# Kernel tuning notes

Hardware: AMD Instinct MI355X
Metric: run time of the kernel (lower is better)

The kernel has to match this reference:

```python
import jax, jax.numpy as jnp
import numpy as np

N_ATOMS = 200_000
N_PAIRS = 20_000_000
N_SPECIES = 4
N_EDGES = 101  # -> 100 bins
R_MAX_GEN = 6.5  # generate some distances beyond the last edge (they are dropped)


def setup_inputs() -> dict:
    key = jax.random.key(0)
    k1, k2, k3, k4 = jax.random.split(key, 4)
    pair_dist = jax.random.uniform(k1, (N_PAIRS,), dtype=jnp.float32) * R_MAX_GEN
    pair_first = jax.random.randint(k2, (N_PAIRS,), 0, N_ATOMS)
    pair_second = jax.random.randint(k3, (N_PAIRS,), 0, N_ATOMS)
    # strict one-hot species encoding per atom (matches hippynn's one_hot input)
    species = jax.random.randint(k4, (N_ATOMS,), 0, N_SPECIES)
    one_hot = species[:, None] == jnp.arange(N_SPECIES)[None, :]
    bins = jnp.linspace(0.0, 6.0, N_EDGES).astype(jnp.float32)  # buffer from __init__
    return {
        "pair_dist": pair_dist,
        "pair_first": pair_first,
        "pair_second": pair_second,
        "one_hot": one_hot,
        "n_molecules": 512,
        "bins": bins,
    }


def reference(pair_dist, pair_first, pair_second, one_hot, n_molecules, bins):
    # Original: for each species pair (i,j), mask pairs where one_hot[pair_first,i]
    # and one_hot[pair_second,j], then histogram masked distances into `bins` via
    # broadcast-compare + diff of counts:  count in bin b = #(bins[b] <= d < bins[b+1]).
    # Fused single-pass equivalent: bucketize each pair distance and scatter-add
    # into a flat (species_i, species_j, bin) histogram.
    n_species = one_hot.shape[-1]
    n_bins = bins.shape[0] - 1

    species = jnp.argmax(one_hot, axis=-1)          # [n_atoms], one-hot -> label
    si = species[pair_first]                        # [n_pairs]
    sj = species[pair_second]                       # [n_pairs]

    # searchsorted(side='right') - 1 gives b s.t. bins[b] <= d < bins[b+1]
    b = jnp.searchsorted(bins, pair_dist, side="right") - 1
    valid = (b >= 0) & (b < n_bins)                 # drop d < bins[0] or d >= bins[-1]
    b_safe = jnp.clip(b, 0, n_bins - 1)

    flat_idx = (si * n_species + sj) * n_bins + b_safe
    weights = valid.astype(pair_dist.dtype)
    rdf = jnp.zeros((n_species * n_species * n_bins,), dtype=pair_dist.dtype)
    rdf = rdf.at[flat_idx].add(weights)
    rdf = rdf.reshape(n_species, n_species, n_bins)
    return (rdf / n_molecules)[None]                # [1, S, S, n_bins]
```

## Files before the change

### kernel.cpp

```cpp
#include <hip/hip_runtime.h>
#include <stdint.h>


#define NSPEC 4
#define HIST_BLOCKS 512

__device__ inline int esize_from_nzw(unsigned int nzw) {
    if (nzw >= 640) return 1;
    if (nzw >= 192) return 4;
    return 8;
}

__device__ inline int get_species(const uint8_t* oh, int atom, int E) {
    if (E == 1) {
        uint32_t v = *(const uint32_t*)(oh + (size_t)atom * 4);
        if (v & 0x000000FFu) return 0;
        if (v & 0x0000FF00u) return 1;
        if (v & 0x00FF0000u) return 2;
        return 3;
    }
    const uint8_t* p = oh + (size_t)atom * 4 * E;
    for (int s = 0; s < NSPEC; ++s) {
        bool nzb = false;
        for (int b = 0; b < E; ++b) nzb |= (p[s * E + b] != 0);
        if (nzb) return s;
    }
    return 0;
}

__global__ void k_species(const uint8_t* __restrict__ oh, int n_atoms,
                          uint32_t* __restrict__ sp2,
                          unsigned int* __restrict__ counts, int n_counts) {
    __shared__ unsigned int s_nz;
    if (threadIdx.x == 0) s_nz = 0;
    __syncthreads();
    unsigned int local = 0;
    #pragma unroll
    for (int k = 0; k < 4; ++k) {
        uint32_t v = ((const uint32_t*)oh)[threadIdx.x * 4 + k];
        local += (v != 0u);
    }
    for (int off = 32; off > 0; off >>= 1) local += __shfl_down(local, off);
    if ((threadIdx.x & 63) == 0) atomicAdd(&s_nz, local);
    __syncthreads();
    const int E = esize_from_nzw(s_nz);

    const int gid = blockIdx.x * blockDim.x + threadIdx.x;
    const int gsz = gridDim.x * blockDim.x;
    for (int j = gid; j < n_counts; j += gsz) counts[j] = 0u;

    const int nw = (n_atoms + 15) >> 4;
    for (int w = gid; w < nw; w += gsz) {
        uint32_t word = 0;
        int base = w << 4;
        int lim = n_atoms - base;
        lim = lim < 16 ? lim : 16;
        for (int k = 0; k < lim; ++k)
            word |= (uint32_t)get_species(oh, base + k, E) << (k * 2);
        sp2[w] = word;
    }
}

__launch_bounds__(1024, 8) __global__
void k_hist_lds(const float* __restrict__ dist, const int* __restrict__ pf,
                const int* __restrict__ ps, const uint32_t* __restrict__ sp2,
                const float* __restrict__ bins, int n_edges, int n_words,
                int npairs, unsigned int* __restrict__ counts,
                unsigned int* __restrict__ part) {
    extern __shared__ float2 smem2[];
    const int n_bins = n_edges - 1;
    const int nh = NSPEC * NSPEC * n_bins;
    float2* eb = smem2;
    uint32_t* tab = (uint32_t*)(eb + n_bins);
    int* h = (int*)(tab + n_words);
    __shared__ int s_exact;

    const int tid = threadIdx.x;
    if (tid == 0) s_exact = 1;
    __syncthreads();

    for (int j = tid; j < n_words; j += blockDim.x) tab[j] = sp2[j];
    for (int j = tid; j < nh + 8; j += blockDim.x) h[j] = 0;
    const float lo = bins[0];
    const float hi = bins[n_edges - 1];
    const float scale = (float)n_bins / (hi - lo);

    for (int j = tid; j < n_edges; j += blockDim.x) {
        float e = bins[j];
        eb[j < n_bins ? j : 0] = make_float2(bins[j < n_bins ? j : 0],
                                             bins[(j < n_bins ? j : 0) + 1]);
        bool ok = true;
        if (j < n_bins) {
            int gi = (int)((e - lo) * scale);
            gi = gi < n_bins - 1 ? gi : n_bins - 1;
            gi = gi > 0 ? gi : 0;
            ok &= (gi == j);
        }
        if (j >= 1) {
            if (e <= 0.f) ok = false;
            else {
                float ep = __int_as_float(__float_as_int(e) - 1);
                int gi = (int)((ep - lo) * scale);
                gi = gi < n_bins - 1 ? gi : n_bins - 1;
                gi = gi > 0 ? gi : 0;
                ok &= (gi == j - 1);
            }
        }
        if (!ok) atomicAnd(&s_exact, 0);
    }
    __syncthreads();

    const int gid = blockIdx.x * blockDim.x + tid;
    const int gsz = gridDim.x * blockDim.x;
    const int nquads = npairs >> 2;
    const int dump = nh + (tid & 7);

    const float4* dist4 = (const float4*)dist;
    const int4* pf4 = (const int4*)pf;
    const int4* ps4 = (const int4*)ps;

    if (s_exact) {
        for (int q = gid; q < nquads; q += gsz) {
            float4 d4 = dist4[q];
            int4 f4 = pf4[q];
            int4 s4 = ps4[q];
            float d[4] = {d4.x, d4.y, d4.z, d4.w};
            int a0[4] = {f4.x, f4.y, f4.z, f4.w};
            int a1[4] = {s4.x, s4.y, s4.z, s4.w};
            uint32_t wi[4], wj[4];
            #pragma unroll
            for (int k = 0; k < 4; ++k) {
                wi[k] = tab[(unsigned)a0[k] >> 4];
                wj[k] = tab[(unsigned)a1[k] >> 4];
            }
            #pragma unroll
            for (int k = 0; k < 4; ++k) {
                int b = (int)((d[k] - lo) * scale);
                b = b < n_bins - 1 ? b : n_bins - 1;
                b = b > 0 ? b : 0;
                int vld = (d[k] >= lo) & (d[k] < hi);
                int si = (int)((wi[k] >> ((a0[k] & 15) << 1)) & 3u);
                int sj = (int)((wj[k] >> ((a1[k] & 15) << 1)) & 3u);
                int idx = (si * NSPEC + sj) * n_bins + b;
                atomicAdd(&h[vld ? idx : dump], 1);
            }
        }
    } else {
        for (int q = gid; q < nquads; q += gsz) {
            float4 d4 = dist4[q];
            int4 f4 = pf4[q];
            int4 s4 = ps4[q];
            float d[4] = {d4.x, d4.y, d4.z, d4.w};
            int a0[4] = {f4.x, f4.y, f4.z, f4.w};
            int a1[4] = {s4.x, s4.y, s4.z, s4.w};
            #pragma unroll
            for (int k = 0; k < 4; ++k) {
                if (d[k] >= lo && d[k] < hi) {
                    int b = (int)((d[k] - lo) * scale);
                    b = b < n_bins - 1 ? b : n_bins - 1;
                    b = b > 0 ? b : 0;
                    while (d[k] < eb[b].x) --b;
                    while (d[k] >= eb[b].y) ++b;
                    int s_i = (int)((tab[(unsigned)a0[k] >> 4] >>
                                     ((a0[k] & 15) << 1)) & 3u);
                    int s_j = (int)((tab[(unsigned)a1[k] >> 4] >>
                                     ((a1[k] & 15) << 1)) & 3u);
                    atomicAdd(&h[(s_i * NSPEC + s_j) * n_bins + b], 1);
                }
            }
        }
    }
    int tail = npairs & 3;
    if (gid < tail) {
        int i = (nquads << 2) + gid;
        float d = dist[i];
        if (d >= lo && d < hi) {
            int b = (int)((d - lo) * scale);
            b = b < n_bins - 1 ? b : n_bins - 1;
            b = b > 0 ? b : 0;
            while (d < eb[b].x) --b;
            while (d >= eb[b].y) ++b;
            int a0 = pf[i], a1 = ps[i];
            int s_i = (int)((tab[(unsigned)a0 >> 4] >> ((a0 & 15) << 1)) & 3u);
            int s_j = (int)((tab[(unsigned)a1 >> 4] >> ((a1 & 15) << 1)) & 3u);
            atomicAdd(&h[(s_i * NSPEC + s_j) * n_bins + b], 1);
        }
    }

    __syncthreads();
    if (part) {
        unsigned int* dst = part + (size_t)blockIdx.x * nh;
        for (int j = tid; j < nh; j += blockDim.x) dst[j] = (unsigned int)h[j];
    } else {
        for (int j = tid; j < nh; j += blockDim.x) {
            int v = h[j];
            if (v) atomicAdd(&counts[j], (unsigned int)v);
        }
    }
}

__launch_bounds__(256, 8) __global__
void k_hist_glb(const float* __restrict__ dist, const int* __restrict__ pf,
                const int* __restrict__ ps, const uint32_t* __restrict__ sp2,
                const float* __restrict__ bins, int n_edges, int npairs,
                unsigned int* __restrict__ counts) {
    const int n_bins = n_edges - 1;
    const int nh = NSPEC * NSPEC * n_bins;
    extern __shared__ float smem[];
    float* sb = smem;
    int* h = (int*)(smem + n_edges);
    const int tid = threadIdx.x;
    for (int j = tid; j < n_edges; j += blockDim.x) sb[j] = bins[j];
    for (int j = tid; j < nh; j += blockDim.x) h[j] = 0;
    __syncthreads();
    const float lo = sb[0];
    const float hi = sb[n_edges - 1];
    const float scale = (float)n_bins / (hi - lo);
    const int gid = blockIdx.x * blockDim.x + tid;
    const int gsz = gridDim.x * blockDim.x;
    auto species_of = [&](int a) -> int {
        return (int)((sp2[a >> 4] >> ((a & 15) << 1)) & 3u);
    };
    auto bin_and_add = [&](float d, int si, int sj) {
        if (d >= lo && d < hi) {
            int b = (int)((d - lo) * scale);
            b = b < n_bins - 1 ? b : n_bins - 1;
            b = b > 0 ? b : 0;
            while (d < sb[b]) --b;
            while (d >= sb[b + 1]) ++b;
            atomicAdd(&h[(si * NSPEC + sj) * n_bins + b], 1);
        }
    };
    const int nquads = npairs >> 2;
    for (int q = gid; q < nquads; q += gsz) {
        float4 d4 = ((const float4*)dist)[q];
        int4 f4 = ((const int4*)pf)[q];
        int4 s4 = ((const int4*)ps)[q];
        bin_and_add(d4.x, species_of(f4.x), species_of(s4.x));
        bin_and_add(d4.y, species_of(f4.y), species_of(s4.y));
        bin_and_add(d4.z, species_of(f4.z), species_of(s4.z));
        bin_and_add(d4.w, species_of(f4.w), species_of(s4.w));
    }
    int tail = npairs & 3;
    if (gid < tail) {
        int i = (nquads << 2) + gid;
        bin_and_add(dist[i], species_of(pf[i]), species_of(ps[i]));
    }
    __syncthreads();
    for (int j = tid; j < nh; j += blockDim.x) {
        int v = h[j];
        if (v) atomicAdd(&counts[j], (unsigned int)v);
    }
}

__global__ void k_reduce(const unsigned int* __restrict__ part, int nblocks,
                         int nh, const int* __restrict__ nmol,
                         float* __restrict__ out) {
    const int tid = threadIdx.x;
    const int bin = blockIdx.x * 32 + (tid >> 3);
    const int sub = tid & 7;
    if (bin >= nh) return;
    unsigned int s = 0;
    for (int k = sub; k < nblocks; k += 8) s += part[(size_t)k * nh + bin];
    s += __shfl_down(s, 4);
    s += __shfl_down(s, 2);
    s += __shfl_down(s, 1);
    if (sub == 0) out[bin] = (float)s / (float)(*nmol);
}

__global__ void k_final(const unsigned int* __restrict__ counts,
                        const int* __restrict__ nmol, float* __restrict__ out,
                        int n) {
    int i = blockIdx.x * blockDim.x + threadIdx.x;
    if (i < n) out[i] = (float)counts[i] / (float)(*nmol);
}

extern "C" void kernel_launch(void* const* d_in, const int* in_sizes, int n_in,
                              void* d_out, int out_size, void* d_ws,
                              size_t ws_size, hipStream_t stream) {
    const float* dist = (const float*)d_in[0];
    const int* pf = (const int*)d_in[1];
    const int* ps = (const int*)d_in[2];
    const uint8_t* oh = (const uint8_t*)d_in[3];
    const int* nmol = (const int*)d_in[4];
    const float* bins = (const float*)d_in[5];
    float* out = (float*)d_out;

    const int npairs = in_sizes[0];
    const int n_edges = in_sizes[5];
    const int n_bins = n_edges - 1;
    const int n_atoms = in_sizes[3] / NSPEC;
    const int nh = NSPEC * NSPEC * n_bins;

    uint8_t* ws = (uint8_t*)d_ws;
    unsigned int* counts = (unsigned int*)ws;
    uint32_t* sp2 = (uint32_t*)(ws + nh * 4 + 64);
    const int n_words = (n_atoms + 15) >> 4;
    size_t part_off = ((size_t)nh * 4 + 64 + (size_t)n_words * 4 + 255) &
                      ~(size_t)255;
    unsigned int* part = (unsigned int*)(ws + part_off);
    const size_t need_part = part_off + (size_t)HIST_BLOCKS * nh * 4;
    const bool use_tree = ws_size >= need_part;

    k_species<<<256, 256, 0, stream>>>(oh, n_atoms, sp2, counts, nh);

    const size_t shmem_lds = (size_t)n_bins * 8 + (size_t)n_words * 4 +
                             (size_t)(nh + 8) * 4;
    if (shmem_lds <= 64 * 1024) {
        k_hist_lds<<<HIST_BLOCKS, 1024, shmem_lds, stream>>>(
            dist, pf, ps, sp2, bins, n_edges, n_words, npairs, counts,
            use_tree ? part : nullptr);
    } else {
        const size_t shmem = (size_t)n_edges * 4 + (size_t)nh * 4;
        k_hist_glb<<<2048, 256, shmem, stream>>>(dist, pf, ps, sp2, bins,
                                                 n_edges, npairs, counts);
    }

    if (use_tree && shmem_lds <= 64 * 1024) {
        k_reduce<<<(nh + 31) / 32, 256, 0, stream>>>(part, HIST_BLOCKS, nh,
                                                     nmol, out);
    } else {
        k_final<<<(out_size + 255) / 256, 256, 0, stream>>>(counts, nmol, out,
                                                            out_size);
    }
}
```

Measured before the change: 89.47 us.

## Software-pipeline histogram loads three deep and drop partial-histogram tree reduction

The exact-binning loop now keeps three rounds of float4/int4 loads in flight in rotating registers, issuing the next round's loads before consuming the current one, so global memory latency overlaps with LDS atomics. Load indices past the end are clamped to the last quad so the prefetch stays in bounds. The per-block partial histogram dump and separate k_reduce kernel are removed in favour of global atomicAdd merging followed by k_final. The edge-pair table fill is also simplified into its own loop. The deeper prefetch raises register pressure, and 512 blocks contending on global atomics may cost more than the tree reduction did.

```diff
diff --git a/kernel.cpp b/kernel.cpp
--- a/kernel.cpp
+++ b/kernel.cpp
@@ -65,8 +65,7 @@
 void k_hist_lds(const float* __restrict__ dist, const int* __restrict__ pf,
                 const int* __restrict__ ps, const uint32_t* __restrict__ sp2,
                 const float* __restrict__ bins, int n_edges, int n_words,
-                int npairs, unsigned int* __restrict__ counts,
-                unsigned int* __restrict__ part) {
+                int npairs, unsigned int* __restrict__ counts) {
     extern __shared__ float2 smem2[];
     const int n_bins = n_edges - 1;
     const int nh = NSPEC * NSPEC * n_bins;
@@ -81,14 +80,14 @@
 
     for (int j = tid; j < n_words; j += blockDim.x) tab[j] = sp2[j];
     for (int j = tid; j < nh + 8; j += blockDim.x) h[j] = 0;
+    for (int j = tid; j < n_bins; j += blockDim.x)
+        eb[j] = make_float2(bins[j], bins[j + 1]);
     const float lo = bins[0];
     const float hi = bins[n_edges - 1];
     const float scale = (float)n_bins / (hi - lo);
 
     for (int j = tid; j < n_edges; j += blockDim.x) {
         float e = bins[j];
-        eb[j < n_bins ? j : 0] = make_float2(bins[j < n_bins ? j : 0],
-                                             bins[(j < n_bins ? j : 0) + 1]);
         bool ok = true;
         if (j < n_bins) {
             int gi = (int)((e - lo) * scale);
@@ -120,31 +119,73 @@
     const int4* ps4 = (const int4*)ps;
 
     if (s_exact) {
-        for (int q = gid; q < nquads; q += gsz) {
-            float4 d4 = dist4[q];
-            int4 f4 = pf4[q];
-            int4 s4 = ps4[q];
-            float d[4] = {d4.x, d4.y, d4.z, d4.w};
-            int a0[4] = {f4.x, f4.y, f4.z, f4.w};
-            int a1[4] = {s4.x, s4.y, s4.z, s4.w};
-            uint32_t wi[4], wj[4];
-            #pragma unroll
-            for (int k = 0; k < 4; ++k) {
-                wi[k] = tab[(unsigned)a0[k] >> 4];
-                wj[k] = tab[(unsigned)a1[k] >> 4];
+        const int last = nquads - 1;
+        int n_iter = 0;
+        if (gid < nquads) n_iter = (nquads - 1 - gid) / gsz + 1;
+
+        float4 dA, dB, dC;
+        int4 fA, fB, fC, sA, sB, sC;
+        int idx = gid;
+
+        #define LD(D, F, S, I)                 \
+            do {                               \
+                int c_ = (I);                  \
+                c_ = c_ < last ? c_ : last;    \
+                D = dist4[c_];                 \
+                F = pf4[c_];                   \
+                S = ps4[c_];                   \
+            } while (0)
+
+        #define CONSUME(D, F, S)                                            \
+            do {                                                            \
+                float d_[4] = {D.x, D.y, D.z, D.w};                         \
+                int a0_[4] = {F.x, F.y, F.z, F.w};                          \
+                int a1_[4] = {S.x, S.y, S.z, S.w};                          \
+                uint32_t wi_[4], wj_[4];                                    \
+                _Pragma("unroll") for (int k = 0; k < 4; ++k) {             \
+                    wi_[k] = tab[(unsigned)a0_[k] >> 4];                    \
+                    wj_[k] = tab[(unsigned)a1_[k] >> 4];                    \
+                }                                                           \
+                _Pragma("unroll") for (int k = 0; k < 4; ++k) {             \
+                    int b_ = (int)((d_[k] - lo) * scale);                   \
+                    b_ = b_ < n_bins - 1 ? b_ : n_bins - 1;                 \
+                    b_ = b_ > 0 ? b_ : 0;                                   \
+                    int vld_ = (d_[k] >= lo) & (d_[k] < hi);                \
+                    int si_ = (int)((wi_[k] >> ((a0_[k] & 15) << 1)) & 3u); \
+                    int sj_ = (int)((wj_[k] >> ((a1_[k] & 15) << 1)) & 3u); \
+                    int hx_ = (si_ * NSPEC + sj_) * n_bins + b_;            \
+                    atomicAdd(&h[vld_ ? hx_ : dump], 1);                    \
+                }                                                           \
+            } while (0)
+
+        if (n_iter > 0) {
+            LD(dA, fA, sA, idx);
+            LD(dB, fB, sB, idx + gsz);
+            LD(dC, fC, sC, idx + 2 * gsz);
+            int it = 0;
+            for (; it + 3 <= n_iter; it += 3) {
+                CONSUME(dA, fA, sA);
+                LD(dA, fA, sA, idx + 3 * gsz);
+                idx += gsz;
+                CONSUME(dB, fB, sB);
+                LD(dB, fB, sB, idx + 3 * gsz);
+                idx += gsz;
+                CONSUME(dC, fC, sC);
+                LD(dC, fC, sC, idx + 3 * gsz);
+                idx += gsz;
             }
-            #pragma unroll
-            for (int k = 0; k < 4; ++k) {
-                int b = (int)((d[k] - lo) * scale);
-                b = b < n_bins - 1 ? b : n_bins - 1;
-                b = b > 0 ? b : 0;
-                int vld = (d[k] >= lo) & (d[k] < hi);
-                int si = (int)((wi[k] >> ((a0[k] & 15) << 1)) & 3u);
-                int sj = (int)((wj[k] >> ((a1[k] & 15) << 1)) & 3u);
-                int idx = (si * NSPEC + sj) * n_bins + b;
-                atomicAdd(&h[vld ? idx : dump], 1);
+            if (it < n_iter) {
+                CONSUME(dA, fA, sA);
+                ++it;
+                if (it < n_iter) {
+                    CONSUME(dB, fB, sB);
+                    ++it;
+                    if (it < n_iter) CONSUME(dC, fC, sC);
+                }
             }
         }
+        #undef LD
+        #undef CONSUME
     } else {
         for (int q = gid; q < nquads; q += gsz) {
             float4 d4 = dist4[q];
@@ -188,14 +229,9 @@
     }
 
     __syncthreads();
-    if (part) {
-        unsigned int* dst = part + (size_t)blockIdx.x * nh;
-        for (int j = tid; j < nh; j += blockDim.x) dst[j] = (unsigned int)h[j];
-    } else {
-        for (int j = tid; j < nh; j += blockDim.x) {
-            int v = h[j];
-            if (v) atomicAdd(&counts[j], (unsigned int)v);
-        }
+    for (int j = tid; j < nh; j += blockDim.x) {
+        int v = h[j];
+        if (v) atomicAdd(&counts[j], (unsigned int)v);
     }
 }
 
@@ -253,21 +289,6 @@
     }
 }
 
-__global__ void k_reduce(const unsigned int* __restrict__ part, int nblocks,
-                         int nh, const int* __restrict__ nmol,
-                         float* __restrict__ out) {
-    const int tid = threadIdx.x;
-    const int bin = blockIdx.x * 32 + (tid >> 3);
-    const int sub = tid & 7;
-    if (bin >= nh) return;
-    unsigned int s = 0;
-    for (int k = sub; k < nblocks; k += 8) s += part[(size_t)k * nh + bin];
-    s += __shfl_down(s, 4);
-    s += __shfl_down(s, 2);
-    s += __shfl_down(s, 1);
-    if (sub == 0) out[bin] = (float)s / (float)(*nmol);
-}
-
 __global__ void k_final(const unsigned int* __restrict__ counts,
                         const int* __restrict__ nmol, float* __restrict__ out,
                         int n) {
@@ -296,11 +317,6 @@
     unsigned int* counts = (unsigned int*)ws;
     uint32_t* sp2 = (uint32_t*)(ws + nh * 4 + 64);
     const int n_words = (n_atoms + 15) >> 4;
-    size_t part_off = ((size_t)nh * 4 + 64 + (size_t)n_words * 4 + 255) &
-                      ~(size_t)255;
-    unsigned int* part = (unsigned int*)(ws + part_off);
-    const size_t need_part = part_off + (size_t)HIST_BLOCKS * nh * 4;
-    const bool use_tree = ws_size >= need_part;
 
     k_species<<<256, 256, 0, stream>>>(oh, n_atoms, sp2, counts, nh);
 
@@ -308,19 +324,13 @@
                              (size_t)(nh + 8) * 4;
     if (shmem_lds <= 64 * 1024) {
         k_hist_lds<<<HIST_BLOCKS, 1024, shmem_lds, stream>>>(
-            dist, pf, ps, sp2, bins, n_edges, n_words, npairs, counts,
-            use_tree ? part : nullptr);
+            dist, pf, ps, sp2, bins, n_edges, n_words, npairs, counts);
     } else {
         const size_t shmem = (size_t)n_edges * 4 + (size_t)nh * 4;
         k_hist_glb<<<2048, 256, shmem, stream>>>(dist, pf, ps, sp2, bins,
                                                  n_edges, npairs, counts);
     }
 
-    if (use_tree && shmem_lds <= 64 * 1024) {
-        k_reduce<<<(nh + 31) / 32, 256, 0, stream>>>(part, HIST_BLOCKS, nh,
-                                                     nmol, out);
-    } else {
-        k_final<<<(out_size + 255) / 256, 256, 0, stream>>>(counts, nmol, out,
-                                                            out_size);
-    }
-}
+    k_final<<<(out_size + 255) / 256, 256, 0, stream>>>(counts, nmol, out,
+                                                        out_size);
+}
```

Result: faster. 80.56 us (-10.0%).

## Fuse final reduction into histogram kernel via last-block atomic counter

Applied to the files above, without the earlier changes.

Replaces the per-block partial histogram write and separate reduce kernel with global atomic accumulation plus a last-block-done counter that writes the normalized output. The main loop now processes two quads per iteration so more loads are in flight, and the edge table setup is simplified. This removes one kernel launch and the partials buffer traffic. In exchange it adds global atomic contention on 1600 counters from 512 blocks and a fence-based completion check.

```diff
diff --git a/kernel.cpp b/kernel.cpp
--- a/kernel.cpp
+++ b/kernel.cpp
@@ -30,7 +30,7 @@
 
 __global__ void k_species(const uint8_t* __restrict__ oh, int n_atoms,
                           uint32_t* __restrict__ sp2,
-                          unsigned int* __restrict__ counts, int n_counts) {
+                          unsigned int* __restrict__ ws_head, int n_counts) {
     __shared__ unsigned int s_nz;
     if (threadIdx.x == 0) s_nz = 0;
     __syncthreads();
@@ -47,7 +47,7 @@
 
     const int gid = blockIdx.x * blockDim.x + threadIdx.x;
     const int gsz = gridDim.x * blockDim.x;
-    for (int j = gid; j < n_counts; j += gsz) counts[j] = 0u;
+    for (int j = gid; j < n_counts + 16; j += gsz) ws_head[j] = 0u;
 
     const int nw = (n_atoms + 15) >> 4;
     for (int w = gid; w < nw; w += gsz) {
@@ -66,7 +66,8 @@
                 const int* __restrict__ ps, const uint32_t* __restrict__ sp2,
                 const float* __restrict__ bins, int n_edges, int n_words,
                 int npairs, unsigned int* __restrict__ counts,
-                unsigned int* __restrict__ part) {
+                unsigned int* __restrict__ done, const int* __restrict__ nmol,
+                float* __restrict__ out) {
     extern __shared__ float2 smem2[];
     const int n_bins = n_edges - 1;
     const int nh = NSPEC * NSPEC * n_bins;
@@ -74,6 +75,7 @@
     uint32_t* tab = (uint32_t*)(eb + n_bins);
     int* h = (int*)(tab + n_words);
     __shared__ int s_exact;
+    __shared__ unsigned int s_rank;
 
     const int tid = threadIdx.x;
     if (tid == 0) s_exact = 1;
@@ -81,14 +83,14 @@
 
     for (int j = tid; j < n_words; j += blockDim.x) tab[j] = sp2[j];
     for (int j = tid; j < nh + 8; j += blockDim.x) h[j] = 0;
+    for (int j = tid; j < n_bins; j += blockDim.x)
+        eb[j] = make_float2(bins[j], bins[j + 1]);
     const float lo = bins[0];
     const float hi = bins[n_edges - 1];
     const float scale = (float)n_bins / (hi - lo);
 
     for (int j = tid; j < n_edges; j += blockDim.x) {
         float e = bins[j];
-        eb[j < n_bins ? j : 0] = make_float2(bins[j < n_bins ? j : 0],
-                                             bins[(j < n_bins ? j : 0) + 1]);
         bool ok = true;
         if (j < n_bins) {
             int gi = (int)((e - lo) * scale);
@@ -113,6 +115,7 @@
     const int gid = blockIdx.x * blockDim.x + tid;
     const int gsz = gridDim.x * blockDim.x;
     const int nquads = npairs >> 2;
+    const int nq2 = nquads >> 1;
     const int dump = nh + (tid & 7);
 
     const float4* dist4 = (const float4*)dist;
@@ -120,24 +123,24 @@
     const int4* ps4 = (const int4*)ps;
 
     if (s_exact) {
-        for (int q = gid; q < nquads; q += gsz) {
-            float4 d4 = dist4[q];
-            int4 f4 = pf4[q];
-            int4 s4 = ps4[q];
-            float d[4] = {d4.x, d4.y, d4.z, d4.w};
-            int a0[4] = {f4.x, f4.y, f4.z, f4.w};
-            int a1[4] = {s4.x, s4.y, s4.z, s4.w};
-            uint32_t wi[4], wj[4];
+        for (int q2 = gid; q2 < nq2; q2 += gsz) {
+            const int q = q2 << 1;
+            float4 dA = dist4[q], dB = dist4[q + 1];
+            int4 fA = pf4[q], fB = pf4[q + 1];
+            int4 sA = ps4[q], sB = ps4[q + 1];
+            float d[8] = {dA.x, dA.y, dA.z, dA.w, dB.x, dB.y, dB.z, dB.w};
+            int a0[8] = {fA.x, fA.y, fA.z, fA.w, fB.x, fB.y, fB.z, fB.w};
+            int a1[8] = {sA.x, sA.y, sA.z, sA.w, sB.x, sB.y, sB.z, sB.w};
+            uint32_t wi[8], wj[8];
             #pragma unroll
-            for (int k = 0; k < 4; ++k) {
+            for (int k = 0; k < 8; ++k) {
                 wi[k] = tab[(unsigned)a0[k] >> 4];
                 wj[k] = tab[(unsigned)a1[k] >> 4];
             }
             #pragma unroll
-            for (int k = 0; k < 4; ++k) {
+            for (int k = 0; k < 8; ++k) {
                 int b = (int)((d[k] - lo) * scale);
-                b = b < n_bins - 1 ? b : n_bins - 1;
-                b = b > 0 ? b : 0;
+                b = min(max(b, 0), n_bins - 1);
                 int vld = (d[k] >= lo) & (d[k] < hi);
                 int si = (int)((wi[k] >> ((a0[k] & 15) << 1)) & 3u);
                 int sj = (int)((wj[k] >> ((a1[k] & 15) << 1)) & 3u);
@@ -146,7 +149,7 @@
             }
         }
     } else {
-        for (int q = gid; q < nquads; q += gsz) {
+        for (int q = gid; q < nq2 << 1; q += gsz) {
             float4 d4 = dist4[q];
             int4 f4 = pf4[q];
             int4 s4 = ps4[q];
@@ -157,8 +160,7 @@
             for (int k = 0; k < 4; ++k) {
                 if (d[k] >= lo && d[k] < hi) {
                     int b = (int)((d[k] - lo) * scale);
-                    b = b < n_bins - 1 ? b : n_bins - 1;
-                    b = b > 0 ? b : 0;
+                    b = min(max(b, 0), n_bins - 1);
                     while (d[k] < eb[b].x) --b;
                     while (d[k] >= eb[b].y) ++b;
                     int s_i = (int)((tab[(unsigned)a0[k] >> 4] >>
@@ -170,31 +172,43 @@
             }
         }
     }
-    int tail = npairs & 3;
-    if (gid < tail) {
-        int i = (nquads << 2) + gid;
-        float d = dist[i];
-        if (d >= lo && d < hi) {
-            int b = (int)((d - lo) * scale);
-            b = b < n_bins - 1 ? b : n_bins - 1;
-            b = b > 0 ? b : 0;
-            while (d < eb[b].x) --b;
-            while (d >= eb[b].y) ++b;
-            int a0 = pf[i], a1 = ps[i];
-            int s_i = (int)((tab[(unsigned)a0 >> 4] >> ((a0 & 15) << 1)) & 3u);
-            int s_j = (int)((tab[(unsigned)a1 >> 4] >> ((a1 & 15) << 1)) & 3u);
-            atomicAdd(&h[(s_i * NSPEC + s_j) * n_bins + b], 1);
-        }
-    }
-
-    __syncthreads();
-    if (part) {
-        unsigned int* dst = part + (size_t)blockIdx.x * nh;
-        for (int j = tid; j < nh; j += blockDim.x) dst[j] = (unsigned int)h[j];
-    } else {
+    {
+        int base = nq2 << 1;
+        int nleft = (nquads - base) * 4 + (npairs & 3);
+        if (gid < nleft) {
+            int i = (base << 2) + gid;
+            float d = dist[i];
+            if (d >= lo && d < hi) {
+                int b = (int)((d - lo) * scale);
+                b = min(max(b, 0), n_bins - 1);
+                while (d < eb[b].x) --b;
+                while (d >= eb[b].y) ++b;
+                int a0 = pf[i], a1 = ps[i];
+                int s_i = (int)((tab[(unsigned)a0 >> 4] >>
+                                 ((a0 & 15) << 1)) & 3u);
+                int s_j = (int)((tab[(unsigned)a1 >> 4] >>
+                                 ((a1 & 15) << 1)) & 3u);
+                atomicAdd(&h[(s_i * NSPEC + s_j) * n_bins + b], 1);
+            }
+        }
+    }
+
+    __syncthreads();
+    for (int j = tid; j < nh; j += blockDim.x) {
+        int v = h[j];
+        if (v) atomicAdd(&counts[j], (unsigned int)v);
+    }
+
+    __threadfence();
+    __syncthreads();
+    if (tid == 0) s_rank = atomicAdd(done, 1u);
+    __syncthreads();
+    if (s_rank == gridDim.x - 1) {
+        __threadfence();
+        const float inv = 1.0f / (float)(*nmol);
         for (int j = tid; j < nh; j += blockDim.x) {
-            int v = h[j];
-            if (v) atomicAdd(&counts[j], (unsigned int)v);
+            unsigned int v = atomicAdd(&counts[j], 0u);
+            out[j] = (float)v * inv;
         }
     }
 }
@@ -224,8 +238,7 @@
     auto bin_and_add = [&](float d, int si, int sj) {
         if (d >= lo && d < hi) {
             int b = (int)((d - lo) * scale);
-            b = b < n_bins - 1 ? b : n_bins - 1;
-            b = b > 0 ? b : 0;
+            b = min(max(b, 0), n_bins - 1);
             while (d < sb[b]) --b;
             while (d >= sb[b + 1]) ++b;
             atomicAdd(&h[(si * NSPEC + sj) * n_bins + b], 1);
@@ -253,21 +266,6 @@
     }
 }
 
-__global__ void k_reduce(const unsigned int* __restrict__ part, int nblocks,
-                         int nh, const int* __restrict__ nmol,
-                         float* __restrict__ out) {
-    const int tid = threadIdx.x;
-    const int bin = blockIdx.x * 32 + (tid >> 3);
-    const int sub = tid & 7;
-    if (bin >= nh) return;
-    unsigned int s = 0;
-    for (int k = sub; k < nblocks; k += 8) s += part[(size_t)k * nh + bin];
-    s += __shfl_down(s, 4);
-    s += __shfl_down(s, 2);
-    s += __shfl_down(s, 1);
-    if (sub == 0) out[bin] = (float)s / (float)(*nmol);
-}
-
 __global__ void k_final(const unsigned int* __restrict__ counts,
                         const int* __restrict__ nmol, float* __restrict__ out,
                         int n) {
@@ -294,13 +292,9 @@
 
     uint8_t* ws = (uint8_t*)d_ws;
     unsigned int* counts = (unsigned int*)ws;
+    unsigned int* done = (unsigned int*)(ws + nh * 4);
     uint32_t* sp2 = (uint32_t*)(ws + nh * 4 + 64);
     const int n_words = (n_atoms + 15) >> 4;
-    size_t part_off = ((size_t)nh * 4 + 64 + (size_t)n_words * 4 + 255) &
-                      ~(size_t)255;
-    unsigned int* part = (unsigned int*)(ws + part_off);
-    const size_t need_part = part_off + (size_t)HIST_BLOCKS * nh * 4;
-    const bool use_tree = ws_size >= need_part;
 
     k_species<<<256, 256, 0, stream>>>(oh, n_atoms, sp2, counts, nh);
 
@@ -308,18 +302,12 @@
                              (size_t)(nh + 8) * 4;
     if (shmem_lds <= 64 * 1024) {
         k_hist_lds<<<HIST_BLOCKS, 1024, shmem_lds, stream>>>(
-            dist, pf, ps, sp2, bins, n_edges, n_words, npairs, counts,
-            use_tree ? part : nullptr);
+            dist, pf, ps, sp2, bins, n_edges, n_words, npairs, counts, done,
+            nmol, out);
     } else {
         const size_t shmem = (size_t)n_edges * 4 + (size_t)nh * 4;
         k_hist_glb<<<2048, 256, shmem, stream>>>(dist, pf, ps, sp2, bins,
                                                  n_edges, npairs, counts);
-    }
-
-    if (use_tree && shmem_lds <= 64 * 1024) {
-        k_reduce<<<(nh + 31) / 32, 256, 0, stream>>>(part, HIST_BLOCKS, nh,
-                                                     nmol, out);
-    } else {
         k_final<<<(out_size + 255) / 256, 256, 0, stream>>>(counts, nmol, out,
                                                             out_size);
     }
```

New measurement: 211.0 us. 136% more time.
